# Kernel optimization log

Hardware: AMD Instinct MI355X
Metric: run time of the kernel (lower is better)

## Reference

```python
import jax, jax.numpy as jnp
import numpy as np

N_NODES = 100000
N_EDGES = 1600000
D_IN = 64
D_H = 64


def setup_inputs() -> dict:
    key = jax.random.key(0)
    ks = jax.random.split(key, 8)
    inp = {
        "in_feat": jax.random.normal(ks[0], (N_NODES, D_IN), dtype=jnp.float32),
        "src": jax.random.randint(ks[1], (N_EDGES,), 0, N_NODES, dtype=jnp.int64)
        if jax.config.jax_enable_x64
        else jax.random.randint(ks[1], (N_EDGES,), 0, N_NODES).astype(jnp.int32),
        "dst": jax.random.randint(ks[2], (N_EDGES,), 0, N_NODES).astype(jnp.int32),
        "W_self1": jax.random.normal(ks[3], (D_H, D_IN), dtype=jnp.float32) * 0.1,
        "W_neigh1": jax.random.normal(ks[4], (D_H, D_IN), dtype=jnp.float32) * 0.1,
        "b1": jnp.zeros((D_H,), dtype=jnp.float32),
        "W_self2": jax.random.normal(ks[5], (D_H, D_H), dtype=jnp.float32) * 0.1,
        "W_neigh2": jax.random.normal(ks[6], (D_H, D_H), dtype=jnp.float32) * 0.1,
        "b2": jnp.zeros((D_H,), dtype=jnp.float32),
    }
    inp["src"] = inp["src"].astype(jnp.int32)
    return inp


def _sage_mean(x, src, dst, W_self, W_neigh, b, n_nodes):
    # mean aggregation over incoming edges: gather src feats, segment-sum at dst
    msg_sum = jax.ops.segment_sum(x[src], dst, num_segments=n_nodes)  # [N, D]
    deg = jax.ops.segment_sum(jnp.ones_like(dst, dtype=x.dtype), dst, num_segments=n_nodes)
    h_neigh = msg_sum / jnp.maximum(deg, 1.0)[:, None]
    # DGL SAGEConv: fc_self(h) + fc_neigh(h_neigh) + bias
    return x @ W_self.T + h_neigh @ W_neigh.T + b


def reference(in_feat, src, dst, W_self1, W_neigh1, b1, W_self2, W_neigh2, b2):
    n = in_feat.shape[0]
    h = _sage_mean(in_feat, src, dst, W_self1, W_neigh1, b1, n)
    # dropout in eval mode is identity; then relu
    h = jax.nn.relu(h)
    h = _sage_mean(h, src, dst, W_self2, W_neigh2, b2, n)
    return h
```

## Files before the change

### kernel.cpp

```cpp
#include <hip/hip_runtime.h>

#define NN 100000
#define NE 1600000
#define NROWS 100032
#define CAP 48
#define ZOFF (NN * 64)
#define NRANGE 12500
#define SCAT_GROUPS 8
#define SCAT_CHUNKS 196
#define SCAT_EPB 8192
#define SCAT_BLKS (SCAT_GROUPS * SCAT_CHUNKS)
#define BINCAP 1536
#define CAST_BLKS 6250
#define WCAT_BLKS 64
#define ZCUR_BLKS 391
#define BIN_BLKS SCAT_CHUNKS
#define AGG_BLKS 1563

typedef __attribute__((ext_vector_type(8))) short short8;
typedef __attribute__((ext_vector_type(4))) float float4v;
typedef __attribute__((ext_vector_type(4))) int int4v;

__device__ inline unsigned short f2bf(float f)
{
    union { float f; unsigned u; } v; v.f = f;
    unsigned r = v.u + 0x7FFF + ((v.u >> 16) & 1);
    return (unsigned short)(r >> 16);
}
__device__ inline float bf2f(unsigned short h)
{
    union { unsigned u; float f; } v; v.u = ((unsigned)h) << 16; return v.f;
}

__global__ __launch_bounds__(256) void zbin_kernel(
    const int* __restrict__ src, const int* __restrict__ dst,
    int* __restrict__ cur, int* __restrict__ bins, int* __restrict__ bcnt)
{
    const int b = blockIdx.x;
    const int tid = threadIdx.x;
    if (b < ZCUR_BLKS) {
        int i = b * 256 + tid;
        if (i < NN) cur[i] = 0;
        return;
    }
    __shared__ int lcnt[8];
    const int c = b - ZCUR_BLKS;
    if (tid < 8) lcnt[tid] = 0;
    __syncthreads();
    const int base = c * SCAT_EPB;
    #pragma unroll
    for (int k = 0; k < 8; ++k) {
        int e = base + (k * 256 + tid) * 4;
        if (e < NE) {
            int4v s4 = __builtin_nontemporal_load((const int4v*)(src + e));
            int4v d4 = __builtin_nontemporal_load((const int4v*)(dst + e));
            #pragma unroll
            for (int r = 0; r < 4; ++r) {
                int d = d4[r];
                int g = (unsigned)d / NRANGE;
                int lpos = atomicAdd(&lcnt[g], 1);
                if (lpos < BINCAP)
                    __builtin_nontemporal_store(
                        ((d - g * NRANGE) << 17) | s4[r],
                        bins + (size_t)(c * 8 + g) * BINCAP + lpos);
            }
        }
    }
    __syncthreads();
    if (tid < 8) bcnt[c * 8 + tid] = min(lcnt[tid], BINCAP);
}

__global__ __launch_bounds__(256) void prep_kernel(
    const float* __restrict__ x,
    const float* __restrict__ Ws1, const float* __restrict__ Wn1,
    const float* __restrict__ Ws2, const float* __restrict__ Wn2,
    const int* __restrict__ bins, const int* __restrict__ bcnt,
    unsigned short* __restrict__ XF,
    unsigned short* __restrict__ W1, unsigned short* __restrict__ W2,
    int* __restrict__ cur, int* __restrict__ colb)
{
    const int b = blockIdx.x;
    const int tid = threadIdx.x;
    if (b < SCAT_BLKS) {
        const int g = b & 7;
        const int c = b >> 3;
        const int lo = g * NRANGE;
        const int m = bcnt[c * 8 + g];
        const int* seg = bins + (size_t)(c * 8 + g) * BINCAP;
        for (int i0 = tid; i0 < m; i0 += 1024) {
            int v[4]; int ok[4];
            #pragma unroll
            for (int r = 0; r < 4; ++r) {
                int idx = i0 + r * 256;
                ok[r] = (idx < m);
                v[r] = ok[r] ? __builtin_nontemporal_load(seg + idx) : 0;
            }
            #pragma unroll
            for (int r = 0; r < 4; ++r) {
                if (ok[r]) {
                    int d = lo + (v[r] >> 17);
                    int s = v[r] & 0x1FFFF;
                    int p = atomicAdd(&cur[d], 1);
                    if (p < CAP) colb[(size_t)d * CAP + p] = s << 6;
                }
            }
        }
    } else if (b < SCAT_BLKS + CAST_BLKS) {
        int t = (b - SCAT_BLKS) * 256 + tid;
        int n = t >> 4;
        int k4 = (t & 15) * 4;
        float4v v = __builtin_nontemporal_load(
            (const float4v*)(x + (size_t)n * 64 + k4));
        ushort4 o;
        o.x = f2bf(v[0]); o.y = f2bf(v[1]); o.z = f2bf(v[2]); o.w = f2bf(v[3]);
        *(ushort4*)(XF + (size_t)n * 64 + k4) = o;
    } else if (b < SCAT_BLKS + CAST_BLKS + WCAT_BLKS) {
        int id = (b - SCAT_BLKS - CAST_BLKS) * 256 + tid;
        int l = id >> 13;
        int r = id & 8191;
        int o = r >> 7, k = r & 127;
        const float* Ws = l ? Ws2 : Ws1;
        const float* Wn = l ? Wn2 : Wn1;
        float v = (k < 64) ? Ws[o * 64 + k] : Wn[o * 64 + (k - 64)];
        (l ? W2 : W1)[r] = f2bf(v);
    } else {
        ushort4 z; z.x = 0; z.y = 0; z.z = 0; z.w = 0;
        for (int i = tid; i < 512; i += 256)
            *(ushort4*)(XF + (size_t)NN * 64 + i * 4) = z;
    }
}

template <int LAYER1>
__global__ __launch_bounds__(256) void aggdense_kernel(
    const unsigned short* __restrict__ XIN,
    const int* __restrict__ cur,
    const int* __restrict__ colb,
    const unsigned short* __restrict__ Wcat,
    const float* __restrict__ bias,
    unsigned short* __restrict__ xout,
    float* __restrict__ fout)
{
    __shared__ __align__(16) unsigned short HN[64 * 72];
    const int tid = threadIdx.x;
    const int wave = tid >> 6;
    const int lane = tid & 63;
    const int g = lane >> 4;
    const int q = lane & 15;
    const int nbase = blockIdx.x * 64 + wave * 16;

    int cntv = (lane < 16 && nbase + lane < NN) ? cur[nbase + lane] : 0;

    int cnt_nx = __shfl(cntv, 0, 64);
    int cc_nx = min(cnt_nx, CAP);
    int ci_nx = (nbase < NN && lane < cc_nx) ? colb[(size_t)nbase * CAP + lane] : ZOFF;

    for (int i = 0; i < 16; ++i) {
        int n = nbase + i;
        int cnt = cnt_nx, cc = cc_nx, ci = ci_nx;
        if (i < 15) {
            cnt_nx = __shfl(cntv, i + 1, 64);
            cc_nx = min(cnt_nx, CAP);
            ci_nx = ((n + 1) < NN && lane < cc_nx)
                      ? colb[(size_t)(n + 1) * CAP + lane] : ZOFF;
        }
        if (n < NN) {
            float a0 = 0.f, a1 = 0.f, a2 = 0.f, a3 = 0.f;
            for (int t = 0; t < cc; t += 16) {
                int i0 = __shfl(ci, t + g, 64);
                int i1 = __shfl(ci, t + 4 + g, 64);
                int i2 = __shfl(ci, t + 8 + g, 64);
                int i3 = __shfl(ci, t + 12 + g, 64);
                ushort4 v0 = *(const ushort4*)(XIN + i0 + q * 4);
                ushort4 v1 = *(const ushort4*)(XIN + i1 + q * 4);
                ushort4 v2 = *(const ushort4*)(XIN + i2 + q * 4);
                ushort4 v3 = *(const ushort4*)(XIN + i3 + q * 4);
                a0 += bf2f(v0.x) + bf2f(v1.x) + bf2f(v2.x) + bf2f(v3.x);
                a1 += bf2f(v0.y) + bf2f(v1.y) + bf2f(v2.y) + bf2f(v3.y);
                a2 += bf2f(v0.z) + bf2f(v1.z) + bf2f(v2.z) + bf2f(v3.z);
                a3 += bf2f(v0.w) + bf2f(v1.w) + bf2f(v2.w) + bf2f(v3.w);
            }
            a0 += __shfl_xor(a0, 16, 64); a0 += __shfl_xor(a0, 32, 64);
            a1 += __shfl_xor(a1, 16, 64); a1 += __shfl_xor(a1, 32, 64);
            a2 += __shfl_xor(a2, 16, 64); a2 += __shfl_xor(a2, 32, 64);
            a3 += __shfl_xor(a3, 16, 64); a3 += __shfl_xor(a3, 32, 64);
            float rdeg = 1.0f / fmaxf((float)cnt, 1.0f);
            if (g == 0) {
                ushort4 o;
                o.x = f2bf(a0 * rdeg); o.y = f2bf(a1 * rdeg);
                o.z = f2bf(a2 * rdeg); o.w = f2bf(a3 * rdeg);
                *(ushort4*)(&HN[(wave * 16 + i) * 72 + q * 4]) = o;
            }
        }
    }
    __syncthreads();

    const int mrow = lane & 15;
    const int kb = lane >> 4;
    const int row0 = nbase;

    short8 a[4];
    {
        const short* ax = (const short*)XIN + (size_t)(row0 + mrow) * 64 + kb * 8;
        const short* ah = (const short*)HN + (wave * 16 + mrow) * 72 + kb * 8;
        a[0] = *(const short8*)(ax);
        a[1] = *(const short8*)(ax + 32);
        a[2] = *(const short8*)(ah);
        a[3] = *(const short8*)(ah + 32);
    }

    float4v acc[4];
    #pragma unroll
    for (int c = 0; c < 4; ++c) acc[c] = (float4v){0.f, 0.f, 0.f, 0.f};

    #pragma unroll
    for (int c = 0; c < 4; ++c) {
        const short* brow = (const short*)Wcat + (c * 16 + mrow) * 128 + kb * 8;
        #pragma unroll
        for (int i = 0; i < 4; ++i) {
            short8 bfr = *(const short8*)(brow + i * 32);
            acc[c] = __builtin_amdgcn_mfma_f32_16x16x32_bf16(a[i], bfr, acc[c], 0, 0, 0);
        }
    }

    const int rbase = row0 + (lane >> 4) * 4;
    #pragma unroll
    for (int c = 0; c < 4; ++c) {
        int o = c * 16 + mrow;
        float bv = bias[o];
        #pragma unroll
        for (int r = 0; r < 4; ++r) {
            int node = rbase + r;
            float val = acc[c][r] + bv;
            if (LAYER1) {
                float h = (node < NN) ? fmaxf(val, 0.f) : 0.f;
                xout[(size_t)node * 64 + o] = f2bf(h);
            } else {
                if (node < NN) fout[(size_t)node * 64 + o] = val;
            }
        }
    }
}

extern "C" void kernel_launch(void* const* d_in, const int* in_sizes, int n_in,
                              void* d_out, int out_size, void* d_ws, size_t ws_size,
                              hipStream_t stream)
{
    const float* in_feat = (const float*)d_in[0];
    const int*   src     = (const int*)d_in[1];
    const int*   dst     = (const int*)d_in[2];
    const float* Ws1     = (const float*)d_in[3];
    const float* Wn1     = (const float*)d_in[4];
    const float* b1      = (const float*)d_in[5];
    const float* Ws2     = (const float*)d_in[6];
    const float* Wn2     = (const float*)d_in[7];
    const float* b2      = (const float*)d_in[8];
    float* out = (float*)d_out;

    int* cur  = (int*)d_ws;
    int* colb = cur + NN;
    unsigned short* XF = (unsigned short*)(colb + (size_t)NN * CAP);
    unsigned short* H1 = XF + (size_t)NROWS * 64;
    unsigned short* W1 = H1 + (size_t)NROWS * 64;
    unsigned short* W2 = W1 + 8192;
    int* bins = (int*)H1;
    int* bcnt = bins + (size_t)BIN_BLKS * 8 * BINCAP;

    zbin_kernel<<<ZCUR_BLKS + BIN_BLKS, 256, 0, stream>>>(src, dst, cur, bins, bcnt);

    prep_kernel<<<SCAT_BLKS + CAST_BLKS + WCAT_BLKS + 1, 256, 0, stream>>>(
        in_feat, Ws1, Wn1, Ws2, Wn2, bins, bcnt, XF, W1, W2, cur, colb);

    aggdense_kernel<1><<<AGG_BLKS, 256, 0, stream>>>(
        XF, cur, colb, W1, b1, H1, nullptr);

    aggdense_kernel<0><<<AGG_BLKS, 256, 0, stream>>>(
        H1, cur, colb, W2, b2, nullptr, out);
}
```

Baseline: 259.7 us.

## Bin edges into fine dst ranges and build CSR with LDS counters

The edge binning now uses 128 narrow destination ranges instead of 8. Each prep block owns one range and counts per-node slots with shared-memory atomics rather than global atomics on cur. The separate cur-zeroing blocks go away because each range block writes its final counts, and the weight cast moves into the binning kernel. The risk is that only 128 blocks do the scatter pass, so parallelism is lower, and bins with fixed capacity 120 could overflow and silently drop edges.

```diff
diff --git a/kernel.cpp b/kernel.cpp
--- a/kernel.cpp
+++ b/kernel.cpp
@@ -5,16 +5,13 @@
 #define NROWS 100032
 #define CAP 48
 #define ZOFF (NN * 64)
-#define NRANGE 12500
-#define SCAT_GROUPS 8
-#define SCAT_CHUNKS 196
+#define NRANGES 128
+#define NRANGE2 782
+#define BINCAP2 120
 #define SCAT_EPB 8192
-#define SCAT_BLKS (SCAT_GROUPS * SCAT_CHUNKS)
-#define BINCAP 1536
+#define NCHUNK 196
 #define CAST_BLKS 6250
 #define WCAT_BLKS 64
-#define ZCUR_BLKS 391
-#define BIN_BLKS SCAT_CHUNKS
 #define AGG_BLKS 1563
 
 typedef __attribute__((ext_vector_type(8))) short short8;
@@ -34,88 +31,42 @@
 
 __global__ __launch_bounds__(256) void zbin_kernel(
     const int* __restrict__ src, const int* __restrict__ dst,
-    int* __restrict__ cur, int* __restrict__ bins, int* __restrict__ bcnt)
+    const float* __restrict__ Ws1, const float* __restrict__ Wn1,
+    const float* __restrict__ Ws2, const float* __restrict__ Wn2,
+    unsigned short* __restrict__ XF,
+    unsigned short* __restrict__ W1, unsigned short* __restrict__ W2,
+    int* __restrict__ bins, int* __restrict__ bcnt)
 {
     const int b = blockIdx.x;
     const int tid = threadIdx.x;
-    if (b < ZCUR_BLKS) {
-        int i = b * 256 + tid;
-        if (i < NN) cur[i] = 0;
-        return;
-    }
-    __shared__ int lcnt[8];
-    const int c = b - ZCUR_BLKS;
-    if (tid < 8) lcnt[tid] = 0;
-    __syncthreads();
-    const int base = c * SCAT_EPB;
-    #pragma unroll
-    for (int k = 0; k < 8; ++k) {
-        int e = base + (k * 256 + tid) * 4;
-        if (e < NE) {
-            int4v s4 = __builtin_nontemporal_load((const int4v*)(src + e));
-            int4v d4 = __builtin_nontemporal_load((const int4v*)(dst + e));
-            #pragma unroll
-            for (int r = 0; r < 4; ++r) {
-                int d = d4[r];
-                int g = (unsigned)d / NRANGE;
-                int lpos = atomicAdd(&lcnt[g], 1);
-                if (lpos < BINCAP)
-                    __builtin_nontemporal_store(
-                        ((d - g * NRANGE) << 17) | s4[r],
-                        bins + (size_t)(c * 8 + g) * BINCAP + lpos);
-            }
-        }
-    }
-    __syncthreads();
-    if (tid < 8) bcnt[c * 8 + tid] = min(lcnt[tid], BINCAP);
-}
-
-__global__ __launch_bounds__(256) void prep_kernel(
-    const float* __restrict__ x,
-    const float* __restrict__ Ws1, const float* __restrict__ Wn1,
-    const float* __restrict__ Ws2, const float* __restrict__ Wn2,
-    const int* __restrict__ bins, const int* __restrict__ bcnt,
-    unsigned short* __restrict__ XF,
-    unsigned short* __restrict__ W1, unsigned short* __restrict__ W2,
-    int* __restrict__ cur, int* __restrict__ colb)
-{
-    const int b = blockIdx.x;
-    const int tid = threadIdx.x;
-    if (b < SCAT_BLKS) {
-        const int g = b & 7;
-        const int c = b >> 3;
-        const int lo = g * NRANGE;
-        const int m = bcnt[c * 8 + g];
-        const int* seg = bins + (size_t)(c * 8 + g) * BINCAP;
-        for (int i0 = tid; i0 < m; i0 += 1024) {
-            int v[4]; int ok[4];
-            #pragma unroll
-            for (int r = 0; r < 4; ++r) {
-                int idx = i0 + r * 256;
-                ok[r] = (idx < m);
-                v[r] = ok[r] ? __builtin_nontemporal_load(seg + idx) : 0;
-            }
-            #pragma unroll
-            for (int r = 0; r < 4; ++r) {
-                if (ok[r]) {
-                    int d = lo + (v[r] >> 17);
-                    int s = v[r] & 0x1FFFF;
-                    int p = atomicAdd(&cur[d], 1);
-                    if (p < CAP) colb[(size_t)d * CAP + p] = s << 6;
+    if (b < NCHUNK) {
+        __shared__ int lcnt[NRANGES];
+        for (int i = tid; i < NRANGES; i += 256) lcnt[i] = 0;
+        __syncthreads();
+        const int base = b * SCAT_EPB;
+        #pragma unroll
+        for (int k = 0; k < 8; ++k) {
+            int e = base + (k * 256 + tid) * 4;
+            if (e < NE) {
+                int4v s4 = __builtin_nontemporal_load((const int4v*)(src + e));
+                int4v d4 = __builtin_nontemporal_load((const int4v*)(dst + e));
+                #pragma unroll
+                for (int r = 0; r < 4; ++r) {
+                    int d = d4[r];
+                    int g = (unsigned)d / NRANGE2;
+                    int lpos = atomicAdd(&lcnt[g], 1);
+                    if (lpos < BINCAP2)
+                        __builtin_nontemporal_store(
+                            ((d - g * NRANGE2) << 17) | s4[r],
+                            bins + (size_t)(b * NRANGES + g) * BINCAP2 + lpos);
                 }
             }
         }
-    } else if (b < SCAT_BLKS + CAST_BLKS) {
-        int t = (b - SCAT_BLKS) * 256 + tid;
-        int n = t >> 4;
-        int k4 = (t & 15) * 4;
-        float4v v = __builtin_nontemporal_load(
-            (const float4v*)(x + (size_t)n * 64 + k4));
-        ushort4 o;
-        o.x = f2bf(v[0]); o.y = f2bf(v[1]); o.z = f2bf(v[2]); o.w = f2bf(v[3]);
-        *(ushort4*)(XF + (size_t)n * 64 + k4) = o;
-    } else if (b < SCAT_BLKS + CAST_BLKS + WCAT_BLKS) {
-        int id = (b - SCAT_BLKS - CAST_BLKS) * 256 + tid;
+        __syncthreads();
+        for (int i = tid; i < NRANGES; i += 256)
+            bcnt[b * NRANGES + i] = min(lcnt[i], BINCAP2);
+    } else if (b < NCHUNK + WCAT_BLKS) {
+        int id = (b - NCHUNK) * 256 + tid;
         int l = id >> 13;
         int r = id & 8191;
         int o = r >> 7, k = r & 127;
@@ -127,6 +78,71 @@
         ushort4 z; z.x = 0; z.y = 0; z.z = 0; z.w = 0;
         for (int i = tid; i < 512; i += 256)
             *(ushort4*)(XF + (size_t)NN * 64 + i * 4) = z;
+    }
+}
+
+__global__ __launch_bounds__(256) void prep_kernel(
+    const float* __restrict__ x,
+    const int* __restrict__ bins, const int* __restrict__ bcnt,
+    unsigned short* __restrict__ XF,
+    int* __restrict__ cur, int* __restrict__ colb)
+{
+    const int b = blockIdx.x;
+    const int tid = threadIdx.x;
+    if (b < NRANGES) {
+        __shared__ int cnt[NRANGE2];
+        const int lo = b * NRANGE2;
+        for (int i = tid; i < NRANGE2; i += 256) cnt[i] = 0;
+        __syncthreads();
+
+        const int grp = tid >> 6;
+        const int i = tid & 63;
+
+        int c = grp;
+        int m = bcnt[c * NRANGES + b];
+        const int* seg = bins + (size_t)(c * NRANGES + b) * BINCAP2;
+        int va = (i < m) ? __builtin_nontemporal_load(seg + i) : -1;
+        int vb = (i + 64 < m) ? __builtin_nontemporal_load(seg + i + 64) : -1;
+
+        for (int cn = grp + 4; cn < NCHUNK; cn += 4) {
+            int m2 = bcnt[cn * NRANGES + b];
+            const int* seg2 = bins + (size_t)(cn * NRANGES + b) * BINCAP2;
+            int wa = (i < m2) ? __builtin_nontemporal_load(seg2 + i) : -1;
+            int wb = (i + 64 < m2) ? __builtin_nontemporal_load(seg2 + i + 64) : -1;
+            if (va >= 0) {
+                int dr = va >> 17;
+                int p = atomicAdd(&cnt[dr], 1);
+                if (p < CAP) colb[(size_t)(lo + dr) * CAP + p] = (va & 0x1FFFF) << 6;
+            }
+            if (vb >= 0) {
+                int dr = vb >> 17;
+                int p = atomicAdd(&cnt[dr], 1);
+                if (p < CAP) colb[(size_t)(lo + dr) * CAP + p] = (vb & 0x1FFFF) << 6;
+            }
+            va = wa; vb = wb;
+        }
+        if (va >= 0) {
+            int dr = va >> 17;
+            int p = atomicAdd(&cnt[dr], 1);
+            if (p < CAP) colb[(size_t)(lo + dr) * CAP + p] = (va & 0x1FFFF) << 6;
+        }
+        if (vb >= 0) {
+            int dr = vb >> 17;
+            int p = atomicAdd(&cnt[dr], 1);
+            if (p < CAP) colb[(size_t)(lo + dr) * CAP + p] = (vb & 0x1FFFF) << 6;
+        }
+        __syncthreads();
+        const int nd = min(NRANGE2, NN - lo);
+        for (int i2 = tid; i2 < nd; i2 += 256) cur[lo + i2] = cnt[i2];
+    } else {
+        int t = (b - NRANGES) * 256 + tid;
+        int n = t >> 4;
+        int k4 = (t & 15) * 4;
+        float4v v = __builtin_nontemporal_load(
+            (const float4v*)(x + (size_t)n * 64 + k4));
+        ushort4 o;
+        o.x = f2bf(v[0]); o.y = f2bf(v[1]); o.z = f2bf(v[2]); o.w = f2bf(v[3]);
+        *(ushort4*)(XF + (size_t)n * 64 + k4) = o;
     }
 }
 
@@ -263,12 +279,13 @@
     unsigned short* W1 = H1 + (size_t)NROWS * 64;
     unsigned short* W2 = W1 + 8192;
     int* bins = (int*)H1;
-    int* bcnt = bins + (size_t)BIN_BLKS * 8 * BINCAP;
-
-    zbin_kernel<<<ZCUR_BLKS + BIN_BLKS, 256, 0, stream>>>(src, dst, cur, bins, bcnt);
-
-    prep_kernel<<<SCAT_BLKS + CAST_BLKS + WCAT_BLKS + 1, 256, 0, stream>>>(
-        in_feat, Ws1, Wn1, Ws2, Wn2, bins, bcnt, XF, W1, W2, cur, colb);
+    int* bcnt = bins + (size_t)NCHUNK * NRANGES * BINCAP2;
+
+    zbin_kernel<<<NCHUNK + WCAT_BLKS + 1, 256, 0, stream>>>(
+        src, dst, Ws1, Wn1, Ws2, Wn2, XF, W1, W2, bins, bcnt);
+
+    prep_kernel<<<NRANGES + CAST_BLKS, 256, 0, stream>>>(
+        in_feat, bins, bcnt, XF, cur, colb);
 
     aggdense_kernel<1><<<AGG_BLKS, 256, 0, stream>>>(
         XF, cur, colb, W1, b1, H1, nullptr);
```

Result: faster. 244.2 us (-5.9%).
